# Kernel tuning notes

Measured on AMD Instinct MI355X. Metric: run time of the kernel, lower is better.

The kernel has to match this reference:

```python
import jax, jax.numpy as jnp
import numpy as np

B, L, D, F_, H = 64, 64, 512, 32, 512  # batch, seq_len, in_dim, fanout, hidden_dim


def setup_inputs() -> dict:
    key = jax.random.key(0)
    ks = jax.random.split(key, 8)
    x = jax.random.normal(ks[0], (B, L, D), dtype=jnp.float32)
    idx1 = jax.random.randint(ks[1], (B, F_), 0, L)          # hop-1 neighbor token ids
    idx2 = jax.random.randint(ks[2], (B, F_ * F_), 0, L)     # hop-2 neighbor token ids
    s_d = 1.0 / np.sqrt(D)
    s_h = 1.0 / np.sqrt(H)
    W_aggr0 = jax.random.normal(ks[3], (D, H), dtype=jnp.float32) * s_d
    b_aggr0 = jnp.zeros((H,), dtype=jnp.float32)
    W_self0 = jax.random.normal(ks[4], (D, H), dtype=jnp.float32) * s_d
    W_aggr1 = jax.random.normal(ks[5], (H, H), dtype=jnp.float32) * s_h
    b_aggr1 = jnp.zeros((H,), dtype=jnp.float32)
    W_self1 = jax.random.normal(ks[6], (H, H), dtype=jnp.float32) * s_h
    return {"x": x, "idx1": idx1, "idx2": idx2,
            "W_aggr0": W_aggr0, "b_aggr0": b_aggr0, "W_self0": W_self0,
            "W_aggr1": W_aggr1, "b_aggr1": b_aggr1, "W_self1": W_self1}


def _sage_gcn(src, nbr, W_aggr, b_aggr, W_self):
    # src: [B, N, d]; nbr: [B, N, F, d]. mean-aggregate + linear, sum with self-transform.
    aggr = jnp.mean(nbr, axis=2) @ W_aggr + b_aggr          # NeighborAggregator('mean')
    return src @ W_self + aggr                               # aggr_hidden_method='sum'


def reference(x, idx1, idx2, W_aggr0, b_aggr0, W_self0, W_aggr1, b_aggr1, W_self1):
    # Gather sampled node features per aspect (level 0 = aspect node itself, index 0).
    f0 = x[:, :1, :]                                               # [B, 1, D]
    f1 = jnp.take_along_axis(x, idx1[:, :, None], axis=1)          # [B, F, D]
    f2 = jnp.take_along_axis(x, idx2[:, :, None], axis=1)          # [B, F*F, D]

    # Layer 0 (shared gcn[0] weights across hops), leaky_relu activation.
    h0 = jax.nn.leaky_relu(_sage_gcn(f0, f1[:, None, :, :], W_aggr0, b_aggr0, W_self0))          # [B,1,H]
    h1 = jax.nn.leaky_relu(_sage_gcn(f1, f2.reshape(B, F_, F_, D), W_aggr0, b_aggr0, W_self0))   # [B,F,H]

    # Layer 1 (gcn[-1], activation=None).
    out = _sage_gcn(h0, h1[:, None, :, :], W_aggr1, b_aggr1, W_self1)                             # [B,1,H]
    return out
```

## Files before the change

kernel.cpp:

```cpp
#include <hip/hip_runtime.h>
#include <hip/hip_bf16.h>

#define B_ 64
#define L_ 64
#define D_ 512
#define F_ 32
#define H_ 512

typedef __attribute__((ext_vector_type(8))) short bf16x8;
typedef __attribute__((ext_vector_type(4))) float f32x4;

__device__ __forceinline__ float leaky(float v) { return v > 0.0f ? v : 0.01f * v; }

__device__ __forceinline__ unsigned short f2bf(float v) {
  unsigned int b = __float_as_uint(v);
  unsigned int r = b + 0x7FFF + ((b >> 16) & 1);
  return (unsigned short)(r >> 16);
}
__device__ __forceinline__ float bf2f(unsigned short h) {
  return __uint_as_float(((unsigned int)h) << 16);
}
__device__ __forceinline__ void cvt_store4(unsigned short* ph, unsigned short* pl, float4 v) {
  ushort4 h, l;
  h.x = f2bf(v.x); l.x = f2bf(v.x - bf2f(h.x));
  h.y = f2bf(v.y); l.y = f2bf(v.y - bf2f(h.y));
  h.z = f2bf(v.z); l.z = f2bf(v.z - bf2f(h.z));
  h.w = f2bf(v.w); l.w = f2bf(v.w - bf2f(h.w));
  *(ushort4*)ph = h;
  *(ushort4*)pl = l;
}

#define GLOAD16(GP, LP)                                              \
  __builtin_amdgcn_global_load_lds(                                  \
      (const __attribute__((address_space(1))) unsigned int*)(GP),   \
      (__attribute__((address_space(3))) unsigned int*)(LP), 16, 0, 0)

__global__ __launch_bounds__(256) void prep(
    const float* __restrict__ x, const int* __restrict__ idx1,
    const int* __restrict__ idx2,
    const float* __restrict__ Ws0, const float* __restrict__ Wa0,
    const float* __restrict__ Ws1, const float* __restrict__ Wa1,
    unsigned short* __restrict__ Xhi, unsigned short* __restrict__ Xlo,
    unsigned short* __restrict__ W0thi, unsigned short* __restrict__ W0tlo,
    unsigned short* __restrict__ W1thi, unsigned short* __restrict__ W1tlo,
    unsigned short* __restrict__ Cm) {
  __shared__ __align__(16) char smem[18432 + 2304];
  const int blk = blockIdx.x;
  const int t = threadIdx.x;

  if (blk < 64) {
    const int b = blk;
    const float* src = x + (size_t)b * (L_ * D_);
    unsigned short* dh = Xhi + (size_t)b * (L_ * D_);
    unsigned short* dl = Xlo + (size_t)b * (L_ * D_);
#pragma unroll 4
    for (int i = 0; i < 32; ++i) {
      const int f4 = t + 256 * i;
      const float4 v = *(const float4*)(src + (size_t)f4 * 4);
      cvt_store4(dh + (size_t)f4 * 4, dl + (size_t)f4 * 4, v);
    }
  } else if (blk < 320) {
    float (*lt)[72] = (float(*)[72])smem;
    const float* src;
    unsigned short *dhi, *dlo;
    int k0, n0, ncol0, dstride;
    if (blk < 192) {
      const int q = blk - 64;
      k0 = (q & 7) * 64;
      n0 = (q >> 3) * 64;
      if (n0 < 512) { src = Ws0; ncol0 = n0; } else { src = Wa0; ncol0 = n0 - 512; }
      dhi = W0thi; dlo = W0tlo; dstride = 512;
    } else {
      const int q = blk - 192;
      k0 = (q & 15) * 64;
      n0 = (q >> 4) * 64;
      if (k0 < 512) { src = Ws1 + (size_t)k0 * H_; } else { src = Wa1 + (size_t)(k0 - 512) * H_; }
      ncol0 = n0; k0 = (blk - 192 & 15) * 64; dhi = W1thi; dlo = W1tlo; dstride = 1024;
    }
    if (blk < 192) {
#pragma unroll
      for (int i = 0; i < 4; ++i) {
        const int idx4 = t + 256 * i;
        const int kl = idx4 >> 4;
        const int n4 = (idx4 & 15) * 4;
        *(float4*)&lt[kl][n4] = *(const float4*)(src + (size_t)(k0 + kl) * H_ + ncol0 + n4);
      }
    } else {
#pragma unroll
      for (int i = 0; i < 4; ++i) {
        const int idx4 = t + 256 * i;
        const int kl = idx4 >> 4;
        const int n4 = (idx4 & 15) * 4;
        *(float4*)&lt[kl][n4] = *(const float4*)(src + (size_t)kl * H_ + ncol0 + n4);
      }
    }
    __syncthreads();
#pragma unroll
    for (int i = 0; i < 4; ++i) {
      const int idx4 = t + 256 * i;
      const int nl = idx4 >> 4;
      const int k4 = (idx4 & 15) * 4;
      ushort4 h, l;
      const float v0 = lt[k4 + 0][nl], v1 = lt[k4 + 1][nl];
      const float v2 = lt[k4 + 2][nl], v3 = lt[k4 + 3][nl];
      h.x = f2bf(v0); l.x = f2bf(v0 - bf2f(h.x));
      h.y = f2bf(v1); l.y = f2bf(v1 - bf2f(h.y));
      h.z = f2bf(v2); l.z = f2bf(v2 - bf2f(h.z));
      h.w = f2bf(v3); l.w = f2bf(v3 - bf2f(h.w));
      *(ushort4*)(dhi + (size_t)(n0 + nl) * dstride + k0 + k4) = h;
      *(ushort4*)(dlo + (size_t)(n0 + nl) * dstride + k0 + k4) = l;
    }
  } else {
    const int b = blk - 320;
    unsigned int* cnt = (unsigned int*)smem;
#pragma unroll
    for (int i = 0; i < 9; ++i) { const int p = t + 256 * i; if (p < 2112) cnt[p] = 0u; }
    __syncthreads();
#pragma unroll
    for (int i = 0; i < 4; ++i) {
      const int j = t + 256 * i;
      atomicAdd(&cnt[(j >> 5) * 64 + idx2[(size_t)b * 1024 + j]], 1u);
    }
    if (t < 32) atomicAdd(&cnt[32 * 64 + idx1[b * F_ + t]], 1u);
    __syncthreads();
#pragma unroll
    for (int i = 0; i < 12; ++i) {
      const int p = t + 256 * i;
      Cm[(size_t)b * 3072 + p] = (p < 2112) ? f2bf((float)cnt[p] * 0.03125f) : (unsigned short)0;
    }
  }
}

__global__ __launch_bounds__(256) void fused1(
    const unsigned short* __restrict__ Xhi, const unsigned short* __restrict__ Xlo,
    const unsigned short* __restrict__ W0thi, const unsigned short* __restrict__ W0tlo,
    const unsigned short* __restrict__ Cm, const int* __restrict__ idx1,
    const float* __restrict__ b0, unsigned short* __restrict__ Hhi,
    unsigned short* __restrict__ Hlo) {
  __shared__ __align__(16) unsigned short lds[24576];
  const int tid = threadIdx.x;
  const int lane = tid & 63;
  const int w = tid >> 6;
  const int wr = w >> 1, wc = w & 1;
  const int lr = lane & 15;
  const int kb = lane >> 4;
  const int rl = lane >> 3;
  const int cbs = ((lane & 7) ^ rl) * 8;

  const int o = blockIdx.x;
  const int b = (o & 7) * 8 + (o >> 6);
  const int s = (o >> 3) & 7;

  f32x4 acc[2][4] = {};

  for (int kt = 0; kt < 8; ++kt) {
    const int kcol = kt * 64 + cbs;
#pragma unroll
    for (int i = 0; i < 12; ++i) {
      const int slot = w * 12 + i;
      const unsigned short* gp;
      int ldsoff;
      if (slot < 8) {
        gp = Xhi + (size_t)(b * 64 + slot * 8 + rl) * 512 + kcol;
        ldsoff = slot * 512;
      } else if (slot < 16) {
        const int u = slot - 8;
        gp = Xlo + (size_t)(b * 64 + u * 8 + rl) * 512 + kcol;
        ldsoff = 4096 + u * 512;
      } else if (slot < 32) {
        const int u = slot - 16;
        const int row = (u >= 8 ? 512 : 0) + s * 64 + (u & 7) * 8 + rl;
        gp = W0thi + (size_t)row * 512 + kcol;
        ldsoff = 8192 + u * 512;
      } else {
        const int u = slot - 32;
        const int row = (u >= 8 ? 512 : 0) + s * 64 + (u & 7) * 8 + rl;
        gp = W0tlo + (size_t)row * 512 + kcol;
        ldsoff = 16384 + u * 512;
      }
      GLOAD16(gp, &lds[ldsoff]);
    }
    __syncthreads();

#define FRG(base, row, CB) \
  (*(const bf16x8*)&lds[(base) + (row) * 64 + (((CB) ^ (lr & 7)) * 8)])
#pragma unroll
    for (int ks = 0; ks < 2; ++ks) {
      const int CB = ks * 4 + kb;
      const bf16x8 Ah0 = FRG(0, wr * 32 + lr, CB);
      const bf16x8 Ah1 = FRG(0, wr * 32 + 16 + lr, CB);
      const bf16x8 Al0 = FRG(4096, wr * 32 + lr, CB);
      const bf16x8 Al1 = FRG(4096, wr * 32 + 16 + lr, CB);
#pragma unroll
      for (int ni = 0; ni < 4; ++ni) {
        const int brow = wc * 64 + ni * 16 + lr;
        const bf16x8 Bh = FRG(8192, brow, CB);
        const bf16x8 Bl = FRG(16384, brow, CB);
        acc[0][ni] = __builtin_amdgcn_mfma_f32_16x16x32_bf16(Ah0, Bh, acc[0][ni], 0, 0, 0);
        acc[0][ni] = __builtin_amdgcn_mfma_f32_16x16x32_bf16(Ah0, Bl, acc[0][ni], 0, 0, 0);
        acc[0][ni] = __builtin_amdgcn_mfma_f32_16x16x32_bf16(Al0, Bh, acc[0][ni], 0, 0, 0);
        acc[1][ni] = __builtin_amdgcn_mfma_f32_16x16x32_bf16(Ah1, Bh, acc[1][ni], 0, 0, 0);
        acc[1][ni] = __builtin_amdgcn_mfma_f32_16x16x32_bf16(Ah1, Bl, acc[1][ni], 0, 0, 0);
        acc[1][ni] = __builtin_amdgcn_mfma_f32_16x16x32_bf16(Al1, Bh, acc[1][ni], 0, 0, 0);
      }
    }
#undef FRG
    __syncthreads();
  }

  float* Ysf = (float*)lds;
  unsigned short* Yh = (unsigned short*)((char*)lds + 17408);
  unsigned short* Yl = Yh + 64 * 72;

  if (wc == 0) {
#pragma unroll
    for (int mi = 0; mi < 2; ++mi)
#pragma unroll
      for (int ni = 0; ni < 4; ++ni)
#pragma unroll
        for (int r = 0; r < 4; ++r) {
          const int row = wr * 32 + mi * 16 + kb * 4 + r;
          const int c = ni * 16 + lr;
          Ysf[row * 68 + c] = acc[mi][ni][r];
        }
  } else {
#pragma unroll
    for (int mi = 0; mi < 2; ++mi)
#pragma unroll
      for (int ni = 0; ni < 4; ++ni)
#pragma unroll
        for (int r = 0; r < 4; ++r) {
          const int row = wr * 32 + mi * 16 + kb * 4 + r;
          const int c = ni * 16 + lr;
          const float v = acc[mi][ni][r];
          const unsigned short h = f2bf(v);
          Yh[c * 72 + row] = h;
          Yl[c * 72 + row] = f2bf(v - bf2f(h));
        }
  }
  __syncthreads();

  bf16x8 Af[3][2];
#pragma unroll
  for (int mi = 0; mi < 3; ++mi)
#pragma unroll
    for (int kf = 0; kf < 2; ++kf)
      Af[mi][kf] = *(const bf16x8*)(Cm + (size_t)b * 3072 + (mi * 16 + lr) * 64 + kf * 32 + kb * 8);

  f32x4 macc[3] = {};
#pragma unroll
  for (int kf = 0; kf < 2; ++kf) {
    const bf16x8 Bh8 = *(const bf16x8*)&Yh[(w * 16 + lr) * 72 + kf * 32 + kb * 8];
    const bf16x8 Bl8 = *(const bf16x8*)&Yl[(w * 16 + lr) * 72 + kf * 32 + kb * 8];
#pragma unroll
    for (int mi = 0; mi < 3; ++mi) {
      macc[mi] = __builtin_amdgcn_mfma_f32_16x16x32_bf16(Af[mi][kf], Bh8, macc[mi], 0, 0, 0);
      macc[mi] = __builtin_amdgcn_mfma_f32_16x16x32_bf16(Af[mi][kf], Bl8, macc[mi], 0, 0, 0);
    }
  }

  const int c = w * 16 + lr;
  const float bias = b0[s * 64 + c];
  float sum = 0.f;
#pragma unroll
  for (int mi = 0; mi < 2; ++mi)
#pragma unroll
    for (int r = 0; r < 4; ++r) {
      const int f = mi * 16 + kb * 4 + r;
      const int xr = idx1[b * F_ + f];
      sum += leaky(Ysf[xr * 68 + c] + macc[mi][r] + bias);
    }
  sum += __shfl_xor(sum, 16);
  sum += __shfl_xor(sum, 32);
  sum *= (1.0f / 32.0f);
  if (lane < 16) {
    unsigned short h = f2bf(sum);
    Hhi[(size_t)b * 1024 + 512 + s * 64 + c] = h;
    Hlo[(size_t)b * 1024 + 512 + s * 64 + c] = f2bf(sum - bf2f(h));
    const float v0 = leaky(Ysf[c] + macc[2][0] + bias);
    const unsigned short h0h = f2bf(v0);
    Hhi[(size_t)b * 1024 + s * 64 + c] = h0h;
    Hlo[(size_t)b * 1024 + s * 64 + c] = f2bf(v0 - bf2f(h0h));
  }
}

__global__ __launch_bounds__(256) void gemm2(
    const unsigned short* __restrict__ Hhi, const unsigned short* __restrict__ Hlo,
    const unsigned short* __restrict__ Wthi, const unsigned short* __restrict__ Wtlo,
    float* __restrict__ part) {
  __shared__ float sacc[256][17];
  const int tid = threadIdx.x;
  const int w = tid >> 6;
  const int lane = tid & 63;
  const int lr = lane & 15;
  const int kb = lane >> 4;
  const int n0 = blockIdx.x * 16;
  const int kc = blockIdx.y * 128;

  f32x4 acc[4] = {};
  const int k = kc + w * 32 + kb * 8;
  const bf16x8 Bh = *(const bf16x8*)(Wthi + (size_t)(n0 + lr) * 1024 + k);
  const bf16x8 Bl = *(const bf16x8*)(Wtlo + (size_t)(n0 + lr) * 1024 + k);
#pragma unroll
  for (int mi = 0; mi < 4; ++mi) {
    const bf16x8 Ah = *(const bf16x8*)(Hhi + (size_t)(mi * 16 + lr) * 1024 + k);
    const bf16x8 Al = *(const bf16x8*)(Hlo + (size_t)(mi * 16 + lr) * 1024 + k);
    acc[mi] = __builtin_amdgcn_mfma_f32_16x16x32_bf16(Ah, Bh, acc[mi], 0, 0, 0);
    acc[mi] = __builtin_amdgcn_mfma_f32_16x16x32_bf16(Ah, Bl, acc[mi], 0, 0, 0);
    acc[mi] = __builtin_amdgcn_mfma_f32_16x16x32_bf16(Al, Bh, acc[mi], 0, 0, 0);
  }
#pragma unroll
  for (int mi = 0; mi < 4; ++mi)
#pragma unroll
    for (int r = 0; r < 4; ++r)
      sacc[((w * 4 + mi) * 4 + kb) * 4 + r][lr] = acc[mi][r];
  __syncthreads();

  const int lr2 = tid & 15;
  const int rg = tid >> 4;
  float* pp = part + (size_t)blockIdx.y * (B_ * H_);
#pragma unroll
  for (int q = 0; q < 4; ++q) {
    const int row = rg * 4 + q;
    const int mi = row >> 4, kb2 = (row >> 2) & 3, r = row & 3;
    float s = 0.f;
#pragma unroll
    for (int w2 = 0; w2 < 4; ++w2)
      s += sacc[((w2 * 4 + mi) * 4 + kb2) * 4 + r][lr2];
    pp[(size_t)row * H_ + n0 + lr2] = s;
  }
}

__global__ __launch_bounds__(256) void reduce_out(
    const float* __restrict__ part, const float* __restrict__ b1,
    float* __restrict__ out) {
  const int idx = blockIdx.x * 256 + threadIdx.x;
  const int c4 = (idx & 127) * 4;
  const size_t off = (size_t)(idx >> 7) * H_ + c4;
  float4 s = *(const float4*)(b1 + c4);
#pragma unroll
  for (int ky = 0; ky < 8; ++ky) {
    const float4 p = *(const float4*)(part + (size_t)ky * (B_ * H_) + off);
    s.x += p.x; s.y += p.y; s.z += p.z; s.w += p.w;
  }
  *(float4*)(out + off) = s;
}

extern "C" void kernel_launch(void* const* d_in, const int* in_sizes, int n_in,
                              void* d_out, int out_size, void* d_ws, size_t ws_size,
                              hipStream_t stream) {
  const float* x    = (const float*)d_in[0];
  const int*   idx1 = (const int*)d_in[1];
  const int*   idx2 = (const int*)d_in[2];
  const float* Wa0  = (const float*)d_in[3];
  const float* b0   = (const float*)d_in[4];
  const float* Ws0  = (const float*)d_in[5];
  const float* Wa1  = (const float*)d_in[6];
  const float* b1   = (const float*)d_in[7];
  const float* Ws1  = (const float*)d_in[8];
  float* out = (float*)d_out;

  unsigned short* wsu = (unsigned short*)d_ws;
  unsigned short* Xhi   = wsu;
  unsigned short* Xlo   = Xhi + (size_t)4096 * 512;
  unsigned short* W0thi = Xlo + (size_t)4096 * 512;
  unsigned short* W0tlo = W0thi + (size_t)1024 * 512;
  unsigned short* W1thi = W0tlo + (size_t)1024 * 512;
  unsigned short* W1tlo = W1thi + (size_t)512 * 1024;
  unsigned short* CmP   = W1tlo + (size_t)512 * 1024;
  unsigned short* Hhi   = CmP + (size_t)64 * 3072;
  unsigned short* Hlo   = Hhi + (size_t)B_ * 1024;
  float* part = (float*)(Hlo + (size_t)B_ * 1024);

  prep<<<384, 256, 0, stream>>>(x, idx1, idx2, Ws0, Wa0, Ws1, Wa1,
                                Xhi, Xlo, W0thi, W0tlo, W1thi, W1tlo, CmP);
  fused1<<<512, 256, 0, stream>>>(Xhi, Xlo, W0thi, W0tlo, CmP, idx1, b0, Hhi, Hlo);
  gemm2<<<dim3(32, 8), 256, 0, stream>>>(Hhi, Hlo, W1thi, W1tlo, part);
  reduce_out<<<32, 256, 0, stream>>>(part, b1, out);
}
```

Baseline: 41.92 us.

## Fuse split-K gemm2 with reduction and widen x conversion grid in prep

The second GEMM now runs as one 512-thread block per 16-column tile. Its eight waves each cover a 128-wide K slice and reduce in shared memory, adding the bias and writing the output directly. This removes the partial-sum buffer round trip and the separate reduce_out launch. In exchange each block does four times the sequential MFMA work, and only 32 blocks run. The prep kernel also spreads the x fp32-to-bf16 hi/lo split across 512 blocks instead of 64, improving memory parallelism.

```diff
diff --git a/kernel.cpp b/kernel.cpp
--- a/kernel.cpp
+++ b/kernel.cpp
@@ -44,55 +44,44 @@
     unsigned short* __restrict__ W0thi, unsigned short* __restrict__ W0tlo,
     unsigned short* __restrict__ W1thi, unsigned short* __restrict__ W1tlo,
     unsigned short* __restrict__ Cm) {
-  __shared__ __align__(16) char smem[18432 + 2304];
+  __shared__ __align__(16) char smem[20736];
   const int blk = blockIdx.x;
   const int t = threadIdx.x;
 
-  if (blk < 64) {
-    const int b = blk;
-    const float* src = x + (size_t)b * (L_ * D_);
-    unsigned short* dh = Xhi + (size_t)b * (L_ * D_);
-    unsigned short* dl = Xlo + (size_t)b * (L_ * D_);
-#pragma unroll 4
-    for (int i = 0; i < 32; ++i) {
-      const int f4 = t + 256 * i;
-      const float4 v = *(const float4*)(src + (size_t)f4 * 4);
-      cvt_store4(dh + (size_t)f4 * 4, dl + (size_t)f4 * 4, v);
-    }
-  } else if (blk < 320) {
+  if (blk < 512) {
+    const int base = blk * 256 + t;
+#pragma unroll
+    for (int i = 0; i < 4; ++i) {
+      const int f4 = base + i * 131072;
+      const float4 v = *(const float4*)(x + (size_t)f4 * 4);
+      cvt_store4(Xhi + (size_t)f4 * 4, Xlo + (size_t)f4 * 4, v);
+    }
+  } else if (blk < 768) {
     float (*lt)[72] = (float(*)[72])smem;
     const float* src;
     unsigned short *dhi, *dlo;
     int k0, n0, ncol0, dstride;
-    if (blk < 192) {
-      const int q = blk - 64;
+    if (blk < 640) {
+      const int q = blk - 512;
       k0 = (q & 7) * 64;
       n0 = (q >> 3) * 64;
       if (n0 < 512) { src = Ws0; ncol0 = n0; } else { src = Wa0; ncol0 = n0 - 512; }
+      src += (size_t)k0 * H_;
       dhi = W0thi; dlo = W0tlo; dstride = 512;
     } else {
-      const int q = blk - 192;
+      const int q = blk - 640;
       k0 = (q & 15) * 64;
       n0 = (q >> 4) * 64;
-      if (k0 < 512) { src = Ws1 + (size_t)k0 * H_; } else { src = Wa1 + (size_t)(k0 - 512) * H_; }
-      ncol0 = n0; k0 = (blk - 192 & 15) * 64; dhi = W1thi; dlo = W1tlo; dstride = 1024;
-    }
-    if (blk < 192) {
-#pragma unroll
-      for (int i = 0; i < 4; ++i) {
-        const int idx4 = t + 256 * i;
-        const int kl = idx4 >> 4;
-        const int n4 = (idx4 & 15) * 4;
-        *(float4*)&lt[kl][n4] = *(const float4*)(src + (size_t)(k0 + kl) * H_ + ncol0 + n4);
-      }
-    } else {
-#pragma unroll
-      for (int i = 0; i < 4; ++i) {
-        const int idx4 = t + 256 * i;
-        const int kl = idx4 >> 4;
-        const int n4 = (idx4 & 15) * 4;
-        *(float4*)&lt[kl][n4] = *(const float4*)(src + (size_t)kl * H_ + ncol0 + n4);
-      }
+      ncol0 = n0;
+      src = (k0 < 512) ? (Ws1 + (size_t)k0 * H_) : (Wa1 + (size_t)(k0 - 512) * H_);
+      dhi = W1thi; dlo = W1tlo; dstride = 1024;
+    }
+#pragma unroll
+    for (int i = 0; i < 4; ++i) {
+      const int idx4 = t + 256 * i;
+      const int kl = idx4 >> 4;
+      const int n4 = (idx4 & 15) * 4;
+      *(float4*)&lt[kl][n4] = *(const float4*)(src + (size_t)kl * H_ + ncol0 + n4);
     }
     __syncthreads();
 #pragma unroll
@@ -111,7 +100,7 @@
       *(ushort4*)(dlo + (size_t)(n0 + nl) * dstride + k0 + k4) = l;
     }
   } else {
-    const int b = blk - 320;
+    const int b = blk - 768;
     unsigned int* cnt = (unsigned int*)smem;
 #pragma unroll
     for (int i = 0; i < 9; ++i) { const int p = t + 256 * i; if (p < 2112) cnt[p] = 0u; }
@@ -284,66 +273,51 @@
   }
 }
 
-__global__ __launch_bounds__(256) void gemm2(
+__global__ __launch_bounds__(512) void gemm2f(
     const unsigned short* __restrict__ Hhi, const unsigned short* __restrict__ Hlo,
     const unsigned short* __restrict__ Wthi, const unsigned short* __restrict__ Wtlo,
-    float* __restrict__ part) {
-  __shared__ float sacc[256][17];
+    const float* __restrict__ b1, float* __restrict__ out) {
+  __shared__ float sacc[8][1088];
   const int tid = threadIdx.x;
   const int w = tid >> 6;
   const int lane = tid & 63;
   const int lr = lane & 15;
   const int kb = lane >> 4;
   const int n0 = blockIdx.x * 16;
-  const int kc = blockIdx.y * 128;
+  const int kc = w * 128;
 
   f32x4 acc[4] = {};
-  const int k = kc + w * 32 + kb * 8;
-  const bf16x8 Bh = *(const bf16x8*)(Wthi + (size_t)(n0 + lr) * 1024 + k);
-  const bf16x8 Bl = *(const bf16x8*)(Wtlo + (size_t)(n0 + lr) * 1024 + k);
-#pragma unroll
-  for (int mi = 0; mi < 4; ++mi) {
-    const bf16x8 Ah = *(const bf16x8*)(Hhi + (size_t)(mi * 16 + lr) * 1024 + k);
-    const bf16x8 Al = *(const bf16x8*)(Hlo + (size_t)(mi * 16 + lr) * 1024 + k);
-    acc[mi] = __builtin_amdgcn_mfma_f32_16x16x32_bf16(Ah, Bh, acc[mi], 0, 0, 0);
-    acc[mi] = __builtin_amdgcn_mfma_f32_16x16x32_bf16(Ah, Bl, acc[mi], 0, 0, 0);
-    acc[mi] = __builtin_amdgcn_mfma_f32_16x16x32_bf16(Al, Bh, acc[mi], 0, 0, 0);
+#pragma unroll
+  for (int ks = 0; ks < 4; ++ks) {
+    const int k = kc + ks * 32 + kb * 8;
+    const bf16x8 Bh = *(const bf16x8*)(Wthi + (size_t)(n0 + lr) * 1024 + k);
+    const bf16x8 Bl = *(const bf16x8*)(Wtlo + (size_t)(n0 + lr) * 1024 + k);
+#pragma unroll
+    for (int mi = 0; mi < 4; ++mi) {
+      const bf16x8 Ah = *(const bf16x8*)(Hhi + (size_t)(mi * 16 + lr) * 1024 + k);
+      const bf16x8 Al = *(const bf16x8*)(Hlo + (size_t)(mi * 16 + lr) * 1024 + k);
+      acc[mi] = __builtin_amdgcn_mfma_f32_16x16x32_bf16(Ah, Bh, acc[mi], 0, 0, 0);
+      acc[mi] = __builtin_amdgcn_mfma_f32_16x16x32_bf16(Ah, Bl, acc[mi], 0, 0, 0);
+      acc[mi] = __builtin_amdgcn_mfma_f32_16x16x32_bf16(Al, Bh, acc[mi], 0, 0, 0);
+    }
   }
 #pragma unroll
   for (int mi = 0; mi < 4; ++mi)
 #pragma unroll
     for (int r = 0; r < 4; ++r)
-      sacc[((w * 4 + mi) * 4 + kb) * 4 + r][lr] = acc[mi][r];
+      sacc[w][(mi * 16 + kb * 4 + r) * 17 + lr] = acc[mi][r];
   __syncthreads();
 
-  const int lr2 = tid & 15;
-  const int rg = tid >> 4;
-  float* pp = part + (size_t)blockIdx.y * (B_ * H_);
-#pragma unroll
-  for (int q = 0; q < 4; ++q) {
-    const int row = rg * 4 + q;
-    const int mi = row >> 4, kb2 = (row >> 2) & 3, r = row & 3;
-    float s = 0.f;
-#pragma unroll
-    for (int w2 = 0; w2 < 4; ++w2)
-      s += sacc[((w2 * 4 + mi) * 4 + kb2) * 4 + r][lr2];
-    pp[(size_t)row * H_ + n0 + lr2] = s;
-  }
-}
-
-__global__ __launch_bounds__(256) void reduce_out(
-    const float* __restrict__ part, const float* __restrict__ b1,
-    float* __restrict__ out) {
-  const int idx = blockIdx.x * 256 + threadIdx.x;
-  const int c4 = (idx & 127) * 4;
-  const size_t off = (size_t)(idx >> 7) * H_ + c4;
-  float4 s = *(const float4*)(b1 + c4);
-#pragma unroll
-  for (int ky = 0; ky < 8; ++ky) {
-    const float4 p = *(const float4*)(part + (size_t)ky * (B_ * H_) + off);
-    s.x += p.x; s.y += p.y; s.z += p.z; s.w += p.w;
-  }
-  *(float4*)(out + off) = s;
+#pragma unroll
+  for (int q = 0; q < 2; ++q) {
+    const int oid = tid * 2 + q;
+    const int row = oid >> 4;
+    const int col = oid & 15;
+    float s = b1[n0 + col];
+#pragma unroll
+    for (int w2 = 0; w2 < 8; ++w2) s += sacc[w2][row * 17 + col];
+    out[(size_t)row * H_ + n0 + col] = s;
+  }
 }
 
 extern "C" void kernel_launch(void* const* d_in, const int* in_sizes, int n_in,
@@ -370,11 +344,9 @@
   unsigned short* CmP   = W1tlo + (size_t)512 * 1024;
   unsigned short* Hhi   = CmP + (size_t)64 * 3072;
   unsigned short* Hlo   = Hhi + (size_t)B_ * 1024;
-  float* part = (float*)(Hlo + (size_t)B_ * 1024);
-
-  prep<<<384, 256, 0, stream>>>(x, idx1, idx2, Ws0, Wa0, Ws1, Wa1,
+
+  prep<<<832, 256, 0, stream>>>(x, idx1, idx2, Ws0, Wa0, Ws1, Wa1,
                                 Xhi, Xlo, W0thi, W0tlo, W1thi, W1tlo, CmP);
   fused1<<<512, 256, 0, stream>>>(Xhi, Xlo, W0thi, W0tlo, CmP, idx1, b0, Hhi, Hlo);
-  gemm2<<<dim3(32, 8), 256, 0, stream>>>(Hhi, Hlo, W1thi, W1tlo, part);
-  reduce_out<<<32, 256, 0, stream>>>(part, b1, out);
-}
+  gemm2f<<<32, 512, 0, stream>>>(Hhi, Hlo, W1thi, W1tlo, b1, out);
+}
```

Measured after the change: 43.26 us. 3.2% more time.
